# Optimization experiments

Measured on AMD Instinct MI355X. Metric: run time of the kernel, lower is better.

## Reference

```python
import jax, jax.numpy as jnp
import numpy as np

B, T, D = 2, 2048, 1024
H, G, K = 16, 4, 64          # num_heads, num_kv_heads, head_dim
R = H // G                   # GQA repeat factor
F = 4096                     # mlp_dim
EPS = 1e-6


def rms_norm(x, scale, eps=EPS):
    var = jnp.mean(x.astype(jnp.float32) ** 2, axis=-1, keepdims=True)
    normed = x * jax.lax.rsqrt(var + eps)
    return (scale * normed).astype(x.dtype)


def apply_rope(x_BTHK, sin_BTK, cos_BTK):
    half = x_BTHK.shape[-1] // 2
    x1, x2 = x_BTHK[..., :half], x_BTHK[..., half:]
    s = sin_BTK[:, :, None, :]
    c = cos_BTK[:, :, None, :]
    return jnp.concatenate([x1 * c - x2 * s, x2 * c + x1 * s], axis=-1).astype(x_BTHK.dtype)


def setup_inputs() -> dict:
    key = jax.random.key(0)
    ks = jax.random.split(key, 12)
    hidden_BTD = jax.random.normal(ks[0], (B, T, D), jnp.float32)
    # rope tables: realistic sin/cos of position*inv_freq
    inv_freq = 1.0 / (10000.0 ** (jnp.arange(K // 2, dtype=jnp.float32) / (K // 2)))
    ang = jnp.arange(T, dtype=jnp.float32)[:, None] * inv_freq[None, :]  # [T, K/2]
    sin_BTK = jnp.broadcast_to(jnp.sin(ang)[None], (B, T, K // 2))
    cos_BTK = jnp.broadcast_to(jnp.cos(ang)[None], (B, T, K // 2))
    mask = jnp.broadcast_to(jnp.tril(jnp.ones((T, T), bool))[None], (B, T, T))
    sc = 1.0 / np.sqrt(D)
    scf = 1.0 / np.sqrt(F)
    return {
        "hidden_BTD": hidden_BTD, "sin_BTK": sin_BTK, "cos_BTK": cos_BTK, "mask": mask,
        "ln1_scale": jnp.ones((D,), jnp.float32),
        "ln2_scale": jnp.ones((D,), jnp.float32),
        "qn_scale": jnp.ones((K,), jnp.float32),
        "kn_scale": jnp.ones((K,), jnp.float32),
        "q_w": jax.random.normal(ks[1], (D, H * K), jnp.float32) * sc,
        "k_w": jax.random.normal(ks[2], (D, G * K), jnp.float32) * sc,
        "v_w": jax.random.normal(ks[3], (D, G * K), jnp.float32) * sc,
        "o_w": jax.random.normal(ks[4], (H * K, D), jnp.float32) * sc,
        "gate_w": jax.random.normal(ks[5], (D, F), jnp.float32) * sc,
        "up_w": jax.random.normal(ks[6], (D, F), jnp.float32) * sc,
        "down_w": jax.random.normal(ks[7], (F, D), jnp.float32) * scf,
    }


def reference(hidden_BTD, sin_BTK, cos_BTK, mask, ln1_scale, ln2_scale,
              qn_scale, kn_scale, q_w, k_w, v_w, o_w, gate_w, up_w, down_w):
    x = rms_norm(hidden_BTD, ln1_scale)
    q = rms_norm((x @ q_w).reshape(B, T, H, K), qn_scale)
    k = rms_norm((x @ k_w).reshape(B, T, G, K), kn_scale)
    v = (x @ v_w).reshape(B, T, G, K)
    q = apply_rope(q, sin_BTK, cos_BTK)
    k = apply_rope(k, sin_BTK, cos_BTK)
    q_BTGRK = q.reshape(B, T, G, R, K)
    scale = K ** (-0.5)
    logits = jnp.einsum('BTGRK,BSGK->BTSGR', q_BTGRK, k) * scale
    neg = float(jnp.finfo(logits.dtype).min)
    logits = jnp.where(mask[:, :, :, None, None], logits, neg)
    weights = jax.nn.softmax(logits.astype(jnp.float32), axis=2).astype(logits.dtype)
    attn = jnp.einsum('BTSGR,BSGK->BTGRK', weights, v).reshape(B, T, H * K)
    hidden_BTD = hidden_BTD + attn @ o_w
    y = rms_norm(hidden_BTD, ln2_scale)
    ff = (jax.nn.silu(y @ gate_w) * (y @ up_w)) @ down_w
    return hidden_BTD + ff
```

## Files before the change

kernel.cpp:

```cpp
#include <hip/hip_runtime.h>
#include <hip/hip_bf16.h>

#define EPSF 1e-6f
constexpr int Bsz  = 2;
constexpr int Tseq = 2048;
constexpr int Dmod = 1024;
constexpr int Hh   = 16;
constexpr int Gg   = 4;
constexpr int Ff   = 4096;
constexpr int Mrows = Bsz * Tseq;

typedef __attribute__((ext_vector_type(8))) short bf16x8;
typedef __attribute__((ext_vector_type(4))) float f32x4;
typedef unsigned short u16;

__device__ inline u16 f2bf(float x) {
    union { float f; unsigned u; } v; v.f = x;
    unsigned r = v.u + 0x7fff + ((v.u >> 16) & 1);
    return (u16)(r >> 16);
}
__device__ inline float bf2f(u16 h) {
    union { unsigned u; float f; } v; v.u = ((unsigned)h) << 16; return v.f;
}

__device__ __forceinline__ void async_copy16(const u16* g, u16* l) {
    __builtin_amdgcn_global_load_lds(
        (const __attribute__((address_space(1))) void*)g,
        (__attribute__((address_space(3))) void*)l, 16, 0, 0);
}


template <int LO>
__global__ __launch_bounds__(256) void wprep_kernel(
    const float* __restrict__ W, u16* __restrict__ Th, u16* __restrict__ Tl,
    int Kd, int N)
{
    __shared__ float tile[32][33];
    const int n0 = blockIdx.x * 32, k0 = blockIdx.y * 32;
    const int r = threadIdx.x >> 3, c4 = (threadIdx.x & 7) * 4;
    const float4 v = *reinterpret_cast<const float4*>(&W[(size_t)(k0 + r) * N + n0 + c4]);
    tile[r][c4 + 0] = v.x; tile[r][c4 + 1] = v.y;
    tile[r][c4 + 2] = v.z; tile[r][c4 + 3] = v.w;
    __syncthreads();
    const int nl = threadIdx.x >> 3, kq = (threadIdx.x & 7) * 4;
    float x0 = tile[kq + 0][nl], x1 = tile[kq + 1][nl];
    float x2 = tile[kq + 2][nl], x3 = tile[kq + 3][nl];
    ushort4 h;
    h.x = f2bf(x0); h.y = f2bf(x1); h.z = f2bf(x2); h.w = f2bf(x3);
    *reinterpret_cast<ushort4*>(&Th[(size_t)(n0 + nl) * Kd + k0 + kq]) = h;
    if (LO) {
        ushort4 l;
        l.x = f2bf(x0 - bf2f(h.x)); l.y = f2bf(x1 - bf2f(h.y));
        l.z = f2bf(x2 - bf2f(h.z)); l.w = f2bf(x3 - bf2f(h.w));
        *reinterpret_cast<ushort4*>(&Tl[(size_t)(n0 + nl) * Kd + k0 + kq]) = l;
    }
}

__global__ __launch_bounds__(256) void wprep_qkv_kernel(
    const float* __restrict__ q_w, const float* __restrict__ k_w,
    const float* __restrict__ v_w, u16* __restrict__ QKVT)
{
    const int nx = blockIdx.x;
    const float* W; int N, n0s, drow;
    if (nx < 32)      { W = q_w; N = 1024; n0s = nx * 32;        drow = nx * 32; }
    else if (nx < 40) { W = k_w; N = 256;  n0s = (nx - 32) * 32; drow = 1024 + (nx - 32) * 32; }
    else              { W = v_w; N = 256;  n0s = (nx - 40) * 32; drow = 1280 + (nx - 40) * 32; }
    const int k0 = blockIdx.y * 32;
    __shared__ float tile[32][33];
    const int r = threadIdx.x >> 3, c4 = (threadIdx.x & 7) * 4;
    const float4 v = *reinterpret_cast<const float4*>(&W[(size_t)(k0 + r) * N + n0s + c4]);
    tile[r][c4 + 0] = v.x; tile[r][c4 + 1] = v.y;
    tile[r][c4 + 2] = v.z; tile[r][c4 + 3] = v.w;
    __syncthreads();
    const int nl = threadIdx.x >> 3, kq = (threadIdx.x & 7) * 4;
    ushort4 h;
    h.x = f2bf(tile[kq + 0][nl]); h.y = f2bf(tile[kq + 1][nl]);
    h.z = f2bf(tile[kq + 2][nl]); h.w = f2bf(tile[kq + 3][nl]);
    *reinterpret_cast<ushort4*>(&QKVT[(size_t)(drow + nl) * 1024 + k0 + kq]) = h;
}

__global__ __launch_bounds__(256) void wprep_gu_kernel(
    const float* __restrict__ gate_w, const float* __restrict__ up_w,
    u16* __restrict__ GTh, u16* __restrict__ UTh)
{
    const float* W = blockIdx.z ? up_w : gate_w;
    u16* T = blockIdx.z ? UTh : GTh;
    const int n0 = blockIdx.x * 32, k0 = blockIdx.y * 32;
    __shared__ float tile[32][33];
    const int r = threadIdx.x >> 3, c4 = (threadIdx.x & 7) * 4;
    const float4 v = *reinterpret_cast<const float4*>(&W[(size_t)(k0 + r) * 4096 + n0 + c4]);
    tile[r][c4 + 0] = v.x; tile[r][c4 + 1] = v.y;
    tile[r][c4 + 2] = v.z; tile[r][c4 + 3] = v.w;
    __syncthreads();
    const int nl = threadIdx.x >> 3, kq = (threadIdx.x & 7) * 4;
    ushort4 h;
    h.x = f2bf(tile[kq + 0][nl]); h.y = f2bf(tile[kq + 1][nl]);
    h.z = f2bf(tile[kq + 2][nl]); h.w = f2bf(tile[kq + 3][nl]);
    *reinterpret_cast<ushort4*>(&T[(size_t)(n0 + nl) * 1024 + k0 + kq]) = h;
}

template <int LO>
__global__ __launch_bounds__(256) void rmsnorm_split_kernel(
    const float* __restrict__ x, const float* __restrict__ scale,
    u16* __restrict__ oh, u16* __restrict__ ol)
{
    const int row = blockIdx.x;
    const int tid = threadIdx.x;
    const float4 v = reinterpret_cast<const float4*>(x + (size_t)row * Dmod)[tid];
    float ss = v.x * v.x + v.y * v.y + v.z * v.z + v.w * v.w;
    #pragma unroll
    for (int off = 32; off; off >>= 1) ss += __shfl_xor(ss, off, 64);
    __shared__ float part[4];
    if ((tid & 63) == 0) part[tid >> 6] = ss;
    __syncthreads();
    const float tot = part[0] + part[1] + part[2] + part[3];
    const float rstd = rsqrtf(tot * (1.0f / Dmod) + EPSF);
    const float4 sc = reinterpret_cast<const float4*>(scale)[tid];
    float o0 = v.x * rstd * sc.x, o1 = v.y * rstd * sc.y;
    float o2 = v.z * rstd * sc.z, o3 = v.w * rstd * sc.w;
    ushort4 h;
    h.x = f2bf(o0); h.y = f2bf(o1); h.z = f2bf(o2); h.w = f2bf(o3);
    *reinterpret_cast<ushort4*>(&oh[(size_t)row * Dmod + tid * 4]) = h;
    if (LO) {
        ushort4 l;
        l.x = f2bf(o0 - bf2f(h.x)); l.y = f2bf(o1 - bf2f(h.y));
        l.z = f2bf(o2 - bf2f(h.z)); l.w = f2bf(o3 - bf2f(h.w));
        *reinterpret_cast<ushort4*>(&ol[(size_t)row * Dmod + tid * 4]) = l;
    }
}

template <int ASPLIT, int BSPLIT, int RES>
__global__ __launch_bounds__(256, 2) void mfma_gemm_kernel(
    const u16* __restrict__ Ah, const u16* __restrict__ Al,
    const u16* __restrict__ Bh, const u16* __restrict__ Bl,
    const float* __restrict__ res, float* __restrict__ C,
    int M, int N, int Kd)
{
    __shared__ u16 As_h[128 * 32];
    __shared__ u16 As_l[128 * 32];
    __shared__ u16 Bs_h[128 * 32];
    __shared__ u16 Bs_l[128 * 32];

    const int tid = threadIdx.x;
    const int lane = tid & 63, wave = tid >> 6;
    const int wm = (wave >> 1) * 64, wn = (wave & 1) * 64;
    const int m0 = blockIdx.y * 128, n0 = blockIdx.x * 128;
    const int fm = lane & 15, quad = lane >> 4;
    const int fsw = (fm >> 1) & 3;
    const int fcol = ((quad ^ fsw) * 8);

    f32x4 acc[4][4];
    #pragma unroll
    for (int i = 0; i < 4; ++i)
        #pragma unroll
        for (int j = 0; j < 4; ++j) acc[i][j] = (f32x4){0.f, 0.f, 0.f, 0.f};

    const int lrow = lane >> 2;
    const int lchunk = lane & 3;
    const int schunk = lchunk ^ ((lrow >> 1) & 3);

    for (int k0 = 0; k0 < Kd; k0 += 32) {
        __syncthreads();
        #pragma unroll
        for (int p = 0; p < 2; ++p) {
            const int row = wave * 32 + p * 16 + lrow;
            const size_t ga = (size_t)(m0 + row) * Kd + k0 + schunk * 8;
            const size_t gb = (size_t)(n0 + row) * Kd + k0 + schunk * 8;
            const int ls = row * 32 + lchunk * 8;
            async_copy16(&Ah[ga], &As_h[ls]);
            if (ASPLIT) async_copy16(&Al[ga], &As_l[ls]);
            async_copy16(&Bh[gb], &Bs_h[ls]);
            if (BSPLIT) async_copy16(&Bl[gb], &Bs_l[ls]);
        }
        __syncthreads();

        bf16x8 ah[4], al[4], bh[4], bl[4];
        #pragma unroll
        for (int t = 0; t < 4; ++t) {
            const int ra = (wm + t * 16 + fm) * 32 + fcol;
            const int rb = (wn + t * 16 + fm) * 32 + fcol;
            ah[t] = *reinterpret_cast<const bf16x8*>(&As_h[ra]);
            bh[t] = *reinterpret_cast<const bf16x8*>(&Bs_h[rb]);
            if (ASPLIT) al[t] = *reinterpret_cast<const bf16x8*>(&As_l[ra]);
            if (BSPLIT) bl[t] = *reinterpret_cast<const bf16x8*>(&Bs_l[rb]);
        }
        #pragma unroll
        for (int mt = 0; mt < 4; ++mt)
            #pragma unroll
            for (int nt = 0; nt < 4; ++nt) {
                acc[mt][nt] = __builtin_amdgcn_mfma_f32_16x16x32_bf16(
                    ah[mt], bh[nt], acc[mt][nt], 0, 0, 0);
                if (BSPLIT)
                    acc[mt][nt] = __builtin_amdgcn_mfma_f32_16x16x32_bf16(
                        ah[mt], bl[nt], acc[mt][nt], 0, 0, 0);
                if (ASPLIT)
                    acc[mt][nt] = __builtin_amdgcn_mfma_f32_16x16x32_bf16(
                        al[mt], bh[nt], acc[mt][nt], 0, 0, 0);
            }
    }

    const int cr = (lane >> 4) * 4, cn = lane & 15;
    #pragma unroll
    for (int mt = 0; mt < 4; ++mt)
        #pragma unroll
        for (int nt = 0; nt < 4; ++nt)
            #pragma unroll
            for (int r = 0; r < 4; ++r) {
                const int gm = m0 + wm + mt * 16 + cr + r;
                const int gn = n0 + wn + nt * 16 + cn;
                float v = acc[mt][nt][r];
                if (RES) v += res[(size_t)gm * N + gn];
                C[(size_t)gm * N + gn] = v;
            }
}

__global__ __launch_bounds__(256, 2) void qkv_fused_kernel(
    const u16* __restrict__ Ah, const u16* __restrict__ Bh,
    const float* __restrict__ qn, const float* __restrict__ kn,
    const float* __restrict__ sinp, const float* __restrict__ cosp,
    u16* __restrict__ Qbh, u16* __restrict__ Qbl,
    u16* __restrict__ Kbh, u16* __restrict__ Kbl,
    u16* __restrict__ Vbh, u16* __restrict__ Vbl)
{
    __shared__ u16 As_h[128 * 32];
    __shared__ u16 Bs_h[128 * 32];

    const int Kd = 1024;
    const int tid = threadIdx.x;
    const int lane = tid & 63, wave = tid >> 6;
    const int wm = (wave >> 1) * 64, wn = (wave & 1) * 64;
    const int m0 = blockIdx.y * 128, n0 = blockIdx.x * 128;
    const int fm = lane & 15, quad = lane >> 4;
    const int fsw = (fm >> 1) & 3;
    const int fcol = ((quad ^ fsw) * 8);

    f32x4 acc[4][4];
    #pragma unroll
    for (int i = 0; i < 4; ++i)
        #pragma unroll
        for (int j = 0; j < 4; ++j) acc[i][j] = (f32x4){0.f, 0.f, 0.f, 0.f};

    const int lrow = lane >> 2;
    const int lchunk = lane & 3;
    const int schunk = lchunk ^ ((lrow >> 1) & 3);

    for (int k0 = 0; k0 < Kd; k0 += 32) {
        __syncthreads();
        #pragma unroll
        for (int p = 0; p < 2; ++p) {
            const int row = wave * 32 + p * 16 + lrow;
            const size_t ga = (size_t)(m0 + row) * Kd + k0 + schunk * 8;
            const size_t gb = (size_t)(n0 + row) * Kd + k0 + schunk * 8;
            const int ls = row * 32 + lchunk * 8;
            async_copy16(&Ah[ga], &As_h[ls]);
            async_copy16(&Bh[gb], &Bs_h[ls]);
        }
        __syncthreads();

        bf16x8 ah[4], bh[4];
        #pragma unroll
        for (int t = 0; t < 4; ++t) {
            ah[t] = *reinterpret_cast<const bf16x8*>(&As_h[(wm + t * 16 + fm) * 32 + fcol]);
            bh[t] = *reinterpret_cast<const bf16x8*>(&Bs_h[(wn + t * 16 + fm) * 32 + fcol]);
        }
        #pragma unroll
        for (int mt = 0; mt < 4; ++mt)
            #pragma unroll
            for (int nt = 0; nt < 4; ++nt)
                acc[mt][nt] = __builtin_amdgcn_mfma_f32_16x16x32_bf16(
                    ah[mt], bh[nt], acc[mt][nt], 0, 0, 0);
    }

    const int gn0 = n0 + wn;
    const int l15 = lane & 15;

    if (gn0 < 1280) {
        const bool isQ = (gn0 < 1024);
        const float* nsc = isQ ? qn : kn;
        const float osc = isQ ? 0.125f : 1.0f;
        u16* __restrict__ oh = isQ ? Qbh : Kbh;
        u16* __restrict__ ol = isQ ? Qbl : Kbl;
        const int rowstride = isQ ? 1024 : 256;
        const int colbase = isQ ? gn0 : gn0 - 1024;
        float sc[4];
        #pragma unroll
        for (int nt = 0; nt < 4; ++nt) sc[nt] = nsc[nt * 16 + l15];

        #pragma unroll
        for (int mt = 0; mt < 4; ++mt)
            #pragma unroll
            for (int r = 0; r < 4; ++r) {
                const int bt = m0 + wm + mt * 16 + quad * 4 + r;
                float v[4];
                #pragma unroll
                for (int nt = 0; nt < 4; ++nt) v[nt] = acc[mt][nt][r];
                float ss = v[0] * v[0] + v[1] * v[1] + v[2] * v[2] + v[3] * v[3];
                #pragma unroll
                for (int off = 1; off < 16; off <<= 1)
                    ss += __shfl_xor(ss, off, 16);
                const float rstd = rsqrtf(ss * (1.0f / 64.0f) + EPSF);
                float nv[4];
                #pragma unroll
                for (int nt = 0; nt < 4; ++nt) nv[nt] = v[nt] * rstd * sc[nt];
                const float s0 = sinp[bt * 32 + l15];
                const float c0 = cosp[bt * 32 + l15];
                const float s1 = sinp[bt * 32 + 16 + l15];
                const float c1 = cosp[bt * 32 + 16 + l15];
                float o[4];
                o[0] = (nv[0] * c0 - nv[2] * s0) * osc;
                o[1] = (nv[1] * c1 - nv[3] * s1) * osc;
                o[2] = (nv[2] * c0 + nv[0] * s0) * osc;
                o[3] = (nv[3] * c1 + nv[1] * s1) * osc;
                #pragma unroll
                for (int nt = 0; nt < 4; ++nt) {
                    const size_t off = (size_t)bt * rowstride + colbase + nt * 16 + l15;
                    const u16 hi = f2bf(o[nt]);
                    oh[off] = hi;
                    ol[off] = f2bf(o[nt] - bf2f(hi));
                }
            }
    } else {
        const int colbase = gn0 - 1280;
        #pragma unroll
        for (int mt = 0; mt < 4; ++mt)
            #pragma unroll
            for (int r = 0; r < 4; ++r) {
                const int bt = m0 + wm + mt * 16 + quad * 4 + r;
                #pragma unroll
                for (int nt = 0; nt < 4; ++nt) {
                    const float v = acc[mt][nt][r];
                    const size_t off = (size_t)bt * 256 + colbase + nt * 16 + l15;
                    const u16 hi = f2bf(v);
                    Vbh[off] = hi;
                    Vbl[off] = f2bf(v - bf2f(hi));
                }
            }
    }
}

__global__ __launch_bounds__(256) void vtrans_bf16_kernel(
    const u16* __restrict__ Vbh, const u16* __restrict__ Vbl,
    u16* __restrict__ Vth, u16* __restrict__ Vtl)
{
    __shared__ u16 th[64 * 66];
    __shared__ u16 tl[64 * 66];
    const int t0 = blockIdx.x * 64;
    const int bg = blockIdx.y;
    const int b = bg >> 2, g = bg & 3;
    const int tid = threadIdx.x;

    const int row = tid >> 2;
    const int cc = (tid & 3) * 16;
    const size_t src = (size_t)(b * Tseq + t0 + row) * 256 + g * 64 + cc;
    *reinterpret_cast<uint4*>(&th[row * 66 + cc]) =
        *reinterpret_cast<const uint4*>(&Vbh[src]);
    *reinterpret_cast<uint4*>(&th[row * 66 + cc + 8]) =
        *reinterpret_cast<const uint4*>(&Vbh[src + 8]);
    *reinterpret_cast<uint4*>(&tl[row * 66 + cc]) =
        *reinterpret_cast<const uint4*>(&Vbl[src]);
    *reinterpret_cast<uint4*>(&tl[row * 66 + cc + 8]) =
        *reinterpret_cast<const uint4*>(&Vbl[src + 8]);
    __syncthreads();

    const int d = tid >> 2;
    const int tq = (tid & 3) * 16;
    u16 oh[16], ol[16];
    #pragma unroll
    for (int i = 0; i < 16; ++i) {
        oh[i] = th[(tq + i) * 66 + d];
        ol[i] = tl[(tq + i) * 66 + d];
    }
    const size_t dst = (size_t)(bg * 64 + d) * Tseq + t0 + tq;
    *reinterpret_cast<uint4*>(&Vth[dst])     = *reinterpret_cast<uint4*>(&oh[0]);
    *reinterpret_cast<uint4*>(&Vth[dst + 8]) = *reinterpret_cast<uint4*>(&oh[8]);
    *reinterpret_cast<uint4*>(&Vtl[dst])     = *reinterpret_cast<uint4*>(&ol[0]);
    *reinterpret_cast<uint4*>(&Vtl[dst + 8]) = *reinterpret_cast<uint4*>(&ol[8]);
}

__global__ __launch_bounds__(256, 2) void mfma_gateup_kernel(
    const u16* __restrict__ Ah, const u16* __restrict__ Al,
    const u16* __restrict__ Bg, const u16* __restrict__ Bu,
    u16* __restrict__ FF, int M, int N, int Kd)
{
    __shared__ u16 As_h[128 * 32];
    __shared__ u16 As_l[128 * 32];
    __shared__ u16 Gs[64 * 32];
    __shared__ u16 Us[64 * 32];

    const int tid = threadIdx.x;
    const int lane = tid & 63, wave = tid >> 6;
    const int wm = (wave >> 1) * 64, wn = (wave & 1) * 32;
    const int m0 = blockIdx.y * 128, n0 = blockIdx.x * 64;
    const int fm = lane & 15, quad = lane >> 4;
    const int fsw = (fm >> 1) & 3;
    const int fcol = ((quad ^ fsw) * 8);

    f32x4 accg[4][2], accu[4][2];
    #pragma unroll
    for (int i = 0; i < 4; ++i)
        #pragma unroll
        for (int j = 0; j < 2; ++j) {
            accg[i][j] = (f32x4){0.f, 0.f, 0.f, 0.f};
            accu[i][j] = (f32x4){0.f, 0.f, 0.f, 0.f};
        }

    const int lrow = lane >> 2;
    const int lchunk = lane & 3;
    const int schunk = lchunk ^ ((lrow >> 1) & 3);

    for (int k0 = 0; k0 < Kd; k0 += 32) {
        __syncthreads();
        #pragma unroll
        for (int p = 0; p < 2; ++p) {
            const int row = p * 64 + wave * 16 + lrow;
            const size_t ga = (size_t)(m0 + row) * Kd + k0 + schunk * 8;
            const int ls = row * 32 + lchunk * 8;
            async_copy16(&Ah[ga], &As_h[ls]);
            async_copy16(&Al[ga], &As_l[ls]);
        }
        {
            const int row = wave * 16 + lrow;
            const size_t gb = (size_t)(n0 + row) * Kd + k0 + schunk * 8;
            const int ls = row * 32 + lchunk * 8;
            async_copy16(&Bg[gb], &Gs[ls]);
            async_copy16(&Bu[gb], &Us[ls]);
        }
        __syncthreads();

        bf16x8 a_h[4], a_l[4], g_f[2], u_f[2];
        #pragma unroll
        for (int t = 0; t < 4; ++t) {
            const int ra = (wm + t * 16 + fm) * 32 + fcol;
            a_h[t] = *reinterpret_cast<const bf16x8*>(&As_h[ra]);
            a_l[t] = *reinterpret_cast<const bf16x8*>(&As_l[ra]);
        }
        #pragma unroll
        for (int j = 0; j < 2; ++j) {
            const int rb = (wn + j * 16 + fm) * 32 + fcol;
            g_f[j] = *reinterpret_cast<const bf16x8*>(&Gs[rb]);
            u_f[j] = *reinterpret_cast<const bf16x8*>(&Us[rb]);
        }
        #pragma unroll
        for (int mt = 0; mt < 4; ++mt)
            #pragma unroll
            for (int nt = 0; nt < 2; ++nt) {
                accg[mt][nt] = __builtin_amdgcn_mfma_f32_16x16x32_bf16(
                    a_h[mt], g_f[nt], accg[mt][nt], 0, 0, 0);
                accg[mt][nt] = __builtin_amdgcn_mfma_f32_16x16x32_bf16(
                    a_l[mt], g_f[nt], accg[mt][nt], 0, 0, 0);
                accu[mt][nt] = __builtin_amdgcn_mfma_f32_16x16x32_bf16(
                    a_h[mt], u_f[nt], accu[mt][nt], 0, 0, 0);
                accu[mt][nt] = __builtin_amdgcn_mfma_f32_16x16x32_bf16(
                    a_l[mt], u_f[nt], accu[mt][nt], 0, 0, 0);
            }
    }

    const int cr = (lane >> 4) * 4, cn = lane & 15;
    #pragma unroll
    for (int mt = 0; mt < 4; ++mt)
        #pragma unroll
        for (int nt = 0; nt < 2; ++nt)
            #pragma unroll
            for (int r = 0; r < 4; ++r) {
                const int gm = m0 + wm + mt * 16 + cr + r;
                const int gn = n0 + wn + nt * 16 + cn;
                const float g = accg[mt][nt][r];
                const float ff = (g / (1.0f + __expf(-g))) * accu[mt][nt][r];
                FF[(size_t)gm * N + gn] = f2bf(ff);
            }
}

__global__ __launch_bounds__(256) void attn_mfma_kernel(
    const u16* __restrict__ Qh, const u16* __restrict__ Ql,
    const u16* __restrict__ Kh, const u16* __restrict__ Kl,
    const u16* __restrict__ Vth, const u16* __restrict__ Vtl,
    u16* __restrict__ AOh, u16* __restrict__ AOl)
{
    __shared__ u16 KsH[64 * 72];
    __shared__ u16 KsL[64 * 72];
    __shared__ u16 VsH[64 * 72];
    __shared__ u16 VsL[64 * 72];
    __shared__ u16 Ps[4][16 * 72];

    const int tid = threadIdx.x;
    const int wave = tid >> 6, lane = tid & 63;
    const int l15 = lane & 15, quad = lane >> 4;

    const int bg = blockIdx.x & 7;
    const int b = bg >> 2, g = bg & 3;
    const int win = 127 - (blockIdx.x >> 3);
    const int t0 = win * 16;
    const int h = g * 4 + wave;

    bf16x8 qh[2], ql[2];
    {
        const size_t qrow = (size_t)(b * Tseq + t0 + l15) * 1024 + h * 64;
        #pragma unroll
        for (int ks = 0; ks < 2; ++ks) {
            qh[ks] = *reinterpret_cast<const bf16x8*>(&Qh[qrow + ks * 32 + quad * 8]);
            ql[ks] = *reinterpret_cast<const bf16x8*>(&Ql[qrow + ks * 32 + quad * 8]);
        }
    }

    const int srow = tid >> 2;
    const int scol = (tid & 3) * 16;
    const size_t kgb = (size_t)(b * Tseq) * 256 + g * 64 + scol;
    const size_t vgb = (size_t)(bg * 64 + srow) * Tseq + scol;

    const int nit = t0 / 64 + 1;

    uint4 ck0, ck1, cl0, cl1, cv0, cv1, cw0, cw1;
    {
        const size_t ka = kgb + (size_t)srow * 256;
        ck0 = *reinterpret_cast<const uint4*>(&Kh[ka]);
        ck1 = *reinterpret_cast<const uint4*>(&Kh[ka + 8]);
        cl0 = *reinterpret_cast<const uint4*>(&Kl[ka]);
        cl1 = *reinterpret_cast<const uint4*>(&Kl[ka + 8]);
        cv0 = *reinterpret_cast<const uint4*>(&Vth[vgb]);
        cv1 = *reinterpret_cast<const uint4*>(&Vth[vgb + 8]);
        cw0 = *reinterpret_cast<const uint4*>(&Vtl[vgb]);
        cw1 = *reinterpret_cast<const uint4*>(&Vtl[vgb + 8]);
    }

    f32x4 oacc[4];
    #pragma unroll
    for (int nt = 0; nt < 4; ++nt) oacc[nt] = (f32x4){0.f, 0.f, 0.f, 0.f};
    float m_r[4], l_r[4];
    #pragma unroll
    for (int r = 0; r < 4; ++r) { m_r[r] = -1e30f; l_r[r] = 0.0f; }

    u16* psw = &Ps[wave][0];
    const int lb = srow * 72 + scol;

    for (int it = 0; it < nit; ++it) {
        const int s0 = it * 64;
        const bool diag = (it == nit - 1);

        __syncthreads();
        *reinterpret_cast<uint4*>(&KsH[lb])     = ck0;
        *reinterpret_cast<uint4*>(&KsH[lb + 8]) = ck1;
        *reinterpret_cast<uint4*>(&KsL[lb])     = cl0;
        *reinterpret_cast<uint4*>(&KsL[lb + 8]) = cl1;
        *reinterpret_cast<uint4*>(&VsH[lb])     = cv0;
        *reinterpret_cast<uint4*>(&VsH[lb + 8]) = cv1;
        *reinterpret_cast<uint4*>(&VsL[lb])     = cw0;
        *reinterpret_cast<uint4*>(&VsL[lb + 8]) = cw1;
        if (it + 1 < nit) {
            const size_t ka = kgb + (size_t)(s0 + 64 + srow) * 256;
            ck0 = *reinterpret_cast<const uint4*>(&Kh[ka]);
            ck1 = *reinterpret_cast<const uint4*>(&Kh[ka + 8]);
            cl0 = *reinterpret_cast<const uint4*>(&Kl[ka]);
            cl1 = *reinterpret_cast<const uint4*>(&Kl[ka + 8]);
            const size_t va = vgb + s0 + 64;
            cv0 = *reinterpret_cast<const uint4*>(&Vth[va]);
            cv1 = *reinterpret_cast<const uint4*>(&Vth[va + 8]);
            cw0 = *reinterpret_cast<const uint4*>(&Vtl[va]);
            cw1 = *reinterpret_cast<const uint4*>(&Vtl[va + 8]);
        }
        __syncthreads();

        f32x4 sacc[4];
        #pragma unroll
        for (int nt = 0; nt < 4; ++nt) sacc[nt] = (f32x4){0.f, 0.f, 0.f, 0.f};

        #pragma unroll
        for (int ks = 0; ks < 2; ++ks) {
            bf16x8 kfh[4], kfl[4];
            #pragma unroll
            for (int nt = 0; nt < 4; ++nt) {
                const int a = (nt * 16 + l15) * 72 + ks * 32 + quad * 8;
                kfh[nt] = *reinterpret_cast<const bf16x8*>(&KsH[a]);
                kfl[nt] = *reinterpret_cast<const bf16x8*>(&KsL[a]);
            }
            #pragma unroll
            for (int nt = 0; nt < 4; ++nt) {
                sacc[nt] = __builtin_amdgcn_mfma_f32_16x16x32_bf16(qh[ks], kfh[nt], sacc[nt], 0, 0, 0);
                sacc[nt] = __builtin_amdgcn_mfma_f32_16x16x32_bf16(ql[ks], kfh[nt], sacc[nt], 0, 0, 0);
                sacc[nt] = __builtin_amdgcn_mfma_f32_16x16x32_bf16(qh[ks], kfl[nt], sacc[nt], 0, 0, 0);
            }
        }

        if (diag) {
            #pragma unroll
            for (int nt = 0; nt < 4; ++nt) {
                const int sg = s0 + nt * 16 + l15;
                #pragma unroll
                for (int r = 0; r < 4; ++r)
                    if (sg > t0 + quad * 4 + r) sacc[nt][r] = -1e30f;
            }
        }

        #pragma unroll
        for (int r = 0; r < 4; ++r) {
            float mx = fmaxf(fmaxf(sacc[0][r], sacc[1][r]),
                             fmaxf(sacc[2][r], sacc[3][r]));
            #pragma unroll
            for (int off = 1; off < 16; off <<= 1)
                mx = fmaxf(mx, __shfl_xor(mx, off, 16));
            const float mnew = fmaxf(m_r[r], mx);
            const float alpha = __expf(m_r[r] - mnew);
            m_r[r] = mnew;

            float rs = 0.0f;
            #pragma unroll
            for (int nt = 0; nt < 4; ++nt) {
                const float p = __expf(sacc[nt][r] - mnew);
                sacc[nt][r] = p;
                rs += p;
            }
            #pragma unroll
            for (int off = 1; off < 16; off <<= 1)
                rs += __shfl_xor(rs, off, 16);
            l_r[r] = l_r[r] * alpha + rs;
            #pragma unroll
            for (int nt = 0; nt < 4; ++nt) oacc[nt][r] *= alpha;
            #pragma unroll
            for (int nt = 0; nt < 4; ++nt)
                psw[(quad * 4 + r) * 72 + nt * 16 + l15] = f2bf(sacc[nt][r]);
        }

        #pragma unroll
        for (int ks = 0; ks < 2; ++ks) {
            const bf16x8 pa = *reinterpret_cast<const bf16x8*>(
                &psw[l15 * 72 + ks * 32 + quad * 8]);
            bf16x8 vfh[4], vfl[4];
            #pragma unroll
            for (int nt = 0; nt < 4; ++nt) {
                const int a = (nt * 16 + l15) * 72 + ks * 32 + quad * 8;
                vfh[nt] = *reinterpret_cast<const bf16x8*>(&VsH[a]);
                vfl[nt] = *reinterpret_cast<const bf16x8*>(&VsL[a]);
            }
            #pragma unroll
            for (int nt = 0; nt < 4; ++nt) {
                oacc[nt] = __builtin_amdgcn_mfma_f32_16x16x32_bf16(pa, vfh[nt], oacc[nt], 0, 0, 0);
                oacc[nt] = __builtin_amdgcn_mfma_f32_16x16x32_bf16(pa, vfl[nt], oacc[nt], 0, 0, 0);
            }
        }
    }

    #pragma unroll
    for (int r = 0; r < 4; ++r) {
        const float inv = 1.0f / l_r[r];
        const size_t orow = (size_t)(b * Tseq + t0 + quad * 4 + r) * 1024 + h * 64;
        #pragma unroll
        for (int nt = 0; nt < 4; ++nt) {
            const float o = oacc[nt][r] * inv;
            const u16 hi = f2bf(o);
            AOh[orow + nt * 16 + l15] = hi;
            AOl[orow + nt * 16 + l15] = f2bf(o - bf2f(hi));
        }
    }
}

extern "C" void kernel_launch(void* const* d_in, const int* in_sizes, int n_in,
                              void* d_out, int out_size, void* d_ws,
                              size_t ws_size, hipStream_t stream)
{
    const float* hidden = (const float*)d_in[0];
    const float* sinp   = (const float*)d_in[1];
    const float* cosp   = (const float*)d_in[2];
    const float* ln1    = (const float*)d_in[4];
    const float* ln2    = (const float*)d_in[5];
    const float* qn     = (const float*)d_in[6];
    const float* kn     = (const float*)d_in[7];
    const float* q_w    = (const float*)d_in[8];
    const float* k_w    = (const float*)d_in[9];
    const float* v_w    = (const float*)d_in[10];
    const float* o_w    = (const float*)d_in[11];
    const float* gate_w = (const float*)d_in[12];
    const float* up_w   = (const float*)d_in[13];
    const float* down_w = (const float*)d_in[14];
    float* out = (float*)d_out;

    char* base = (char*)d_ws;
    u16*   OTh  = (u16*)(base);
    u16*   OTl  = (u16*)(base + 2097152);
    u16*   GTh  = (u16*)(base + 4194304);
    u16*   UTh  = (u16*)(base + 12582912);
    u16*   DTh  = (u16*)(base + 20971520);
    u16*   QKVT = (u16*)(base + 29360128);
    u16*   Xh   = (u16*)(base + 32505856);
    u16*   Qbh  = (u16*)(base + 40894464);
    u16*   Qbl  = (u16*)(base + 49283072);
    u16*   Kbh  = (u16*)(base + 57671680);
    u16*   Kbl  = (u16*)(base + 59768832);
    u16*   Vbh  = (u16*)(base + 61865984);
    u16*   Vbl  = (u16*)(base + 63963136);
    u16*   Vth  = (u16*)(base + 66060288);
    u16*   Vtl  = (u16*)(base + 68157440);
    u16*   AOh  = (u16*)(base + 70254592);
    u16*   AOl  = (u16*)(base + 78643200);
    u16*   FFh  = (u16*)(base + 87031808);

    float* H2 = (float*)Qbh;
    u16*   Yh = Kbh;
    u16*   Yl = Vth;

    wprep_qkv_kernel<<<dim3(48, 32), 256, 0, stream>>>(q_w, k_w, v_w, QKVT);
    wprep_kernel<1><<<dim3(32, 32), 256, 0, stream>>>(o_w, OTh, OTl, 1024, 1024);
    wprep_gu_kernel<<<dim3(128, 32, 2), 256, 0, stream>>>(gate_w, up_w, GTh, UTh);
    wprep_kernel<0><<<dim3(32, 128), 256, 0, stream>>>(down_w, DTh, nullptr, 4096, 1024);

    rmsnorm_split_kernel<0><<<Mrows, 256, 0, stream>>>(hidden, ln1, Xh, nullptr);

    qkv_fused_kernel<<<dim3(12, 32), 256, 0, stream>>>(
        Xh, QKVT, qn, kn, sinp, cosp, Qbh, Qbl, Kbh, Kbl, Vbh, Vbl);

    vtrans_bf16_kernel<<<dim3(Tseq / 64, Bsz * Gg), 256, 0, stream>>>(
        Vbh, Vbl, Vth, Vtl);

    attn_mfma_kernel<<<Bsz * Gg * (Tseq / 16), 256, 0, stream>>>(
        Qbh, Qbl, Kbh, Kbl, Vth, Vtl, AOh, AOl);

    mfma_gemm_kernel<1, 1, 1><<<dim3(8, 32), 256, 0, stream>>>(
        AOh, AOl, OTh, OTl, hidden, H2, Mrows, Dmod, 1024);

    rmsnorm_split_kernel<1><<<Mrows, 256, 0, stream>>>(H2, ln2, Yh, Yl);

    mfma_gateup_kernel<<<dim3(Ff / 64, Mrows / 128), 256, 0, stream>>>(
        Yh, Yl, GTh, UTh, FFh, Mrows, Ff, 1024);

    mfma_gemm_kernel<0, 0, 1><<<dim3(8, 32), 256, 0, stream>>>(
        FFh, nullptr, DTh, nullptr, H2, out, Mrows, Dmod, 4096);
}
```

Measured before the change: 543.8 us.

## Merge weight-prep kernels, write V transposed from QKV, process two query strips per attention block

Folds the four weight conversion kernels into one launch over a flat block index, removing launch overhead. The QKV GEMM epilogue now writes V directly in the transposed layout, dropping the separate V transpose kernel and its round trip through memory. The attention kernel handles two 16-row query strips per block so each staged K/V tile is reused twice, halving the grid and K/V traffic. In exchange it raises register pressure in attention and uses strided 8-byte stores for V.

```diff
diff --git a/kernel.cpp b/kernel.cpp
--- a/kernel.cpp
+++ b/kernel.cpp
@@ -30,13 +30,48 @@
 }
 
 
-template <int LO>
-__global__ __launch_bounds__(256) void wprep_kernel(
-    const float* __restrict__ W, u16* __restrict__ Th, u16* __restrict__ Tl,
-    int Kd, int N)
+__global__ __launch_bounds__(256) void wprep_all_kernel(
+    const float* __restrict__ q_w, const float* __restrict__ k_w,
+    const float* __restrict__ v_w, const float* __restrict__ o_w,
+    const float* __restrict__ gate_w, const float* __restrict__ up_w,
+    const float* __restrict__ down_w,
+    u16* __restrict__ QKVT, u16* __restrict__ OTh, u16* __restrict__ OTl,
+    u16* __restrict__ GTh, u16* __restrict__ UTh, u16* __restrict__ DTh)
 {
+    const int bx = blockIdx.x;
+    const float* W; u16* Th; u16* Tl = nullptr;
+    int N, Kd, ntile, ktile, drow;
+    if (bx < 1024) {
+        W = q_w; N = 1024; Kd = 1024; ntile = bx & 31; ktile = bx >> 5;
+        Th = QKVT; drow = ntile * 32;
+    } else if (bx < 1280) {
+        const int i = bx - 1024;
+        W = k_w; N = 256; Kd = 1024; ntile = i & 7; ktile = i >> 3;
+        Th = QKVT; drow = 1024 + ntile * 32;
+    } else if (bx < 1536) {
+        const int i = bx - 1280;
+        W = v_w; N = 256; Kd = 1024; ntile = i & 7; ktile = i >> 3;
+        Th = QKVT; drow = 1280 + ntile * 32;
+    } else if (bx < 2560) {
+        const int i = bx - 1536;
+        W = o_w; N = 1024; Kd = 1024; ntile = i & 31; ktile = i >> 5;
+        Th = OTh; Tl = OTl; drow = ntile * 32;
+    } else if (bx < 6656) {
+        const int i = bx - 2560;
+        W = gate_w; N = 4096; Kd = 1024; ntile = i & 127; ktile = i >> 7;
+        Th = GTh; drow = ntile * 32;
+    } else if (bx < 10752) {
+        const int i = bx - 6656;
+        W = up_w; N = 4096; Kd = 1024; ntile = i & 127; ktile = i >> 7;
+        Th = UTh; drow = ntile * 32;
+    } else {
+        const int i = bx - 10752;
+        W = down_w; N = 1024; Kd = 4096; ntile = i & 31; ktile = i >> 5;
+        Th = DTh; drow = ntile * 32;
+    }
+    const int n0 = ntile * 32, k0 = ktile * 32;
+
     __shared__ float tile[32][33];
-    const int n0 = blockIdx.x * 32, k0 = blockIdx.y * 32;
     const int r = threadIdx.x >> 3, c4 = (threadIdx.x & 7) * 4;
     const float4 v = *reinterpret_cast<const float4*>(&W[(size_t)(k0 + r) * N + n0 + c4]);
     tile[r][c4 + 0] = v.x; tile[r][c4 + 1] = v.y;
@@ -47,56 +82,13 @@
     float x2 = tile[kq + 2][nl], x3 = tile[kq + 3][nl];
     ushort4 h;
     h.x = f2bf(x0); h.y = f2bf(x1); h.z = f2bf(x2); h.w = f2bf(x3);
-    *reinterpret_cast<ushort4*>(&Th[(size_t)(n0 + nl) * Kd + k0 + kq]) = h;
-    if (LO) {
+    *reinterpret_cast<ushort4*>(&Th[(size_t)(drow + nl) * Kd + k0 + kq]) = h;
+    if (Tl) {
         ushort4 l;
         l.x = f2bf(x0 - bf2f(h.x)); l.y = f2bf(x1 - bf2f(h.y));
         l.z = f2bf(x2 - bf2f(h.z)); l.w = f2bf(x3 - bf2f(h.w));
-        *reinterpret_cast<ushort4*>(&Tl[(size_t)(n0 + nl) * Kd + k0 + kq]) = l;
-    }
-}
-
-__global__ __launch_bounds__(256) void wprep_qkv_kernel(
-    const float* __restrict__ q_w, const float* __restrict__ k_w,
-    const float* __restrict__ v_w, u16* __restrict__ QKVT)
-{
-    const int nx = blockIdx.x;
-    const float* W; int N, n0s, drow;
-    if (nx < 32)      { W = q_w; N = 1024; n0s = nx * 32;        drow = nx * 32; }
-    else if (nx < 40) { W = k_w; N = 256;  n0s = (nx - 32) * 32; drow = 1024 + (nx - 32) * 32; }
-    else              { W = v_w; N = 256;  n0s = (nx - 40) * 32; drow = 1280 + (nx - 40) * 32; }
-    const int k0 = blockIdx.y * 32;
-    __shared__ float tile[32][33];
-    const int r = threadIdx.x >> 3, c4 = (threadIdx.x & 7) * 4;
-    const float4 v = *reinterpret_cast<const float4*>(&W[(size_t)(k0 + r) * N + n0s + c4]);
-    tile[r][c4 + 0] = v.x; tile[r][c4 + 1] = v.y;
-    tile[r][c4 + 2] = v.z; tile[r][c4 + 3] = v.w;
-    __syncthreads();
-    const int nl = threadIdx.x >> 3, kq = (threadIdx.x & 7) * 4;
-    ushort4 h;
-    h.x = f2bf(tile[kq + 0][nl]); h.y = f2bf(tile[kq + 1][nl]);
-    h.z = f2bf(tile[kq + 2][nl]); h.w = f2bf(tile[kq + 3][nl]);
-    *reinterpret_cast<ushort4*>(&QKVT[(size_t)(drow + nl) * 1024 + k0 + kq]) = h;
-}
-
-__global__ __launch_bounds__(256) void wprep_gu_kernel(
-    const float* __restrict__ gate_w, const float* __restrict__ up_w,
-    u16* __restrict__ GTh, u16* __restrict__ UTh)
-{
-    const float* W = blockIdx.z ? up_w : gate_w;
-    u16* T = blockIdx.z ? UTh : GTh;
-    const int n0 = blockIdx.x * 32, k0 = blockIdx.y * 32;
-    __shared__ float tile[32][33];
-    const int r = threadIdx.x >> 3, c4 = (threadIdx.x & 7) * 4;
-    const float4 v = *reinterpret_cast<const float4*>(&W[(size_t)(k0 + r) * 4096 + n0 + c4]);
-    tile[r][c4 + 0] = v.x; tile[r][c4 + 1] = v.y;
-    tile[r][c4 + 2] = v.z; tile[r][c4 + 3] = v.w;
-    __syncthreads();
-    const int nl = threadIdx.x >> 3, kq = (threadIdx.x & 7) * 4;
-    ushort4 h;
-    h.x = f2bf(tile[kq + 0][nl]); h.y = f2bf(tile[kq + 1][nl]);
-    h.z = f2bf(tile[kq + 2][nl]); h.w = f2bf(tile[kq + 3][nl]);
-    *reinterpret_cast<ushort4*>(&T[(size_t)(n0 + nl) * 1024 + k0 + kq]) = h;
+        *reinterpret_cast<ushort4*>(&Tl[(size_t)(drow + nl) * Kd + k0 + kq]) = l;
+    }
 }
 
 template <int LO>
@@ -220,7 +212,7 @@
     const float* __restrict__ sinp, const float* __restrict__ cosp,
     u16* __restrict__ Qbh, u16* __restrict__ Qbl,
     u16* __restrict__ Kbh, u16* __restrict__ Kbl,
-    u16* __restrict__ Vbh, u16* __restrict__ Vbl)
+    u16* __restrict__ Vth, u16* __restrict__ Vtl)
 {
     __shared__ u16 As_h[128 * 32];
     __shared__ u16 Bs_h[128 * 32];
@@ -320,61 +312,25 @@
                 }
             }
     } else {
-        const int colbase = gn0 - 1280;
+        const int g = (gn0 - 1280) >> 6;
+        const int b = (m0 + wm) >> 11;
+        const int tb = ((m0 + wm) & 2047) + quad * 4;
         #pragma unroll
         for (int mt = 0; mt < 4; ++mt)
             #pragma unroll
-            for (int r = 0; r < 4; ++r) {
-                const int bt = m0 + wm + mt * 16 + quad * 4 + r;
-                #pragma unroll
-                for (int nt = 0; nt < 4; ++nt) {
-                    const float v = acc[mt][nt][r];
-                    const size_t off = (size_t)bt * 256 + colbase + nt * 16 + l15;
-                    const u16 hi = f2bf(v);
-                    Vbh[off] = hi;
-                    Vbl[off] = f2bf(v - bf2f(hi));
-                }
+            for (int nt = 0; nt < 4; ++nt) {
+                const float v0 = acc[mt][nt][0], v1 = acc[mt][nt][1];
+                const float v2 = acc[mt][nt][2], v3 = acc[mt][nt][3];
+                ushort4 hv, lv;
+                hv.x = f2bf(v0); hv.y = f2bf(v1); hv.z = f2bf(v2); hv.w = f2bf(v3);
+                lv.x = f2bf(v0 - bf2f(hv.x)); lv.y = f2bf(v1 - bf2f(hv.y));
+                lv.z = f2bf(v2 - bf2f(hv.z)); lv.w = f2bf(v3 - bf2f(hv.w));
+                const size_t off =
+                    ((size_t)((b * 4 + g) * 64 + nt * 16 + l15)) * Tseq + tb + mt * 16;
+                *reinterpret_cast<ushort4*>(&Vth[off]) = hv;
+                *reinterpret_cast<ushort4*>(&Vtl[off]) = lv;
             }
     }
-}
-
-__global__ __launch_bounds__(256) void vtrans_bf16_kernel(
-    const u16* __restrict__ Vbh, const u16* __restrict__ Vbl,
-    u16* __restrict__ Vth, u16* __restrict__ Vtl)
-{
-    __shared__ u16 th[64 * 66];
-    __shared__ u16 tl[64 * 66];
-    const int t0 = blockIdx.x * 64;
-    const int bg = blockIdx.y;
-    const int b = bg >> 2, g = bg & 3;
-    const int tid = threadIdx.x;
-
-    const int row = tid >> 2;
-    const int cc = (tid & 3) * 16;
-    const size_t src = (size_t)(b * Tseq + t0 + row) * 256 + g * 64 + cc;
-    *reinterpret_cast<uint4*>(&th[row * 66 + cc]) =
-        *reinterpret_cast<const uint4*>(&Vbh[src]);
-    *reinterpret_cast<uint4*>(&th[row * 66 + cc + 8]) =
-        *reinterpret_cast<const uint4*>(&Vbh[src + 8]);
-    *reinterpret_cast<uint4*>(&tl[row * 66 + cc]) =
-        *reinterpret_cast<const uint4*>(&Vbl[src]);
-    *reinterpret_cast<uint4*>(&tl[row * 66 + cc + 8]) =
-        *reinterpret_cast<const uint4*>(&Vbl[src + 8]);
-    __syncthreads();
-
-    const int d = tid >> 2;
-    const int tq = (tid & 3) * 16;
-    u16 oh[16], ol[16];
-    #pragma unroll
-    for (int i = 0; i < 16; ++i) {
-        oh[i] = th[(tq + i) * 66 + d];
-        ol[i] = tl[(tq + i) * 66 + d];
-    }
-    const size_t dst = (size_t)(bg * 64 + d) * Tseq + t0 + tq;
-    *reinterpret_cast<uint4*>(&Vth[dst])     = *reinterpret_cast<uint4*>(&oh[0]);
-    *reinterpret_cast<uint4*>(&Vth[dst + 8]) = *reinterpret_cast<uint4*>(&oh[8]);
-    *reinterpret_cast<uint4*>(&Vtl[dst])     = *reinterpret_cast<uint4*>(&ol[0]);
-    *reinterpret_cast<uint4*>(&Vtl[dst + 8]) = *reinterpret_cast<uint4*>(&ol[8]);
 }
 
 __global__ __launch_bounds__(256, 2) void mfma_gateup_kernel(
@@ -470,6 +426,91 @@
             }
 }
 
+__device__ __forceinline__ void attn_strip_step(
+    const bf16x8* qh, const bf16x8* ql,
+    const u16* KsH, const u16* KsL, const u16* VsH, const u16* VsL,
+    u16* psw, int s0, int t0, int l15, int quad,
+    f32x4* oacc, float* m_r, float* l_r)
+{
+    f32x4 sacc[4];
+    #pragma unroll
+    for (int nt = 0; nt < 4; ++nt) sacc[nt] = (f32x4){0.f, 0.f, 0.f, 0.f};
+
+    #pragma unroll
+    for (int ks = 0; ks < 2; ++ks) {
+        bf16x8 kfh[4], kfl[4];
+        #pragma unroll
+        for (int nt = 0; nt < 4; ++nt) {
+            const int a = (nt * 16 + l15) * 72 + ks * 32 + quad * 8;
+            kfh[nt] = *reinterpret_cast<const bf16x8*>(&KsH[a]);
+            kfl[nt] = *reinterpret_cast<const bf16x8*>(&KsL[a]);
+        }
+        #pragma unroll
+        for (int nt = 0; nt < 4; ++nt) {
+            sacc[nt] = __builtin_amdgcn_mfma_f32_16x16x32_bf16(qh[ks], kfh[nt], sacc[nt], 0, 0, 0);
+            sacc[nt] = __builtin_amdgcn_mfma_f32_16x16x32_bf16(ql[ks], kfh[nt], sacc[nt], 0, 0, 0);
+            sacc[nt] = __builtin_amdgcn_mfma_f32_16x16x32_bf16(qh[ks], kfl[nt], sacc[nt], 0, 0, 0);
+        }
+    }
+
+    if (s0 + 63 > t0) {
+        #pragma unroll
+        for (int nt = 0; nt < 4; ++nt) {
+            const int sg = s0 + nt * 16 + l15;
+            #pragma unroll
+            for (int r = 0; r < 4; ++r)
+                if (sg > t0 + quad * 4 + r) sacc[nt][r] = -1e30f;
+        }
+    }
+
+    #pragma unroll
+    for (int r = 0; r < 4; ++r) {
+        float mx = fmaxf(fmaxf(sacc[0][r], sacc[1][r]),
+                         fmaxf(sacc[2][r], sacc[3][r]));
+        #pragma unroll
+        for (int off = 1; off < 16; off <<= 1)
+            mx = fmaxf(mx, __shfl_xor(mx, off, 16));
+        const float mnew = fmaxf(m_r[r], mx);
+        const float alpha = __expf(m_r[r] - mnew);
+        m_r[r] = mnew;
+
+        float rs = 0.0f;
+        #pragma unroll
+        for (int nt = 0; nt < 4; ++nt) {
+            const float p = __expf(sacc[nt][r] - mnew);
+            sacc[nt][r] = p;
+            rs += p;
+        }
+        #pragma unroll
+        for (int off = 1; off < 16; off <<= 1)
+            rs += __shfl_xor(rs, off, 16);
+        l_r[r] = l_r[r] * alpha + rs;
+        #pragma unroll
+        for (int nt = 0; nt < 4; ++nt) oacc[nt][r] *= alpha;
+        #pragma unroll
+        for (int nt = 0; nt < 4; ++nt)
+            psw[(quad * 4 + r) * 72 + nt * 16 + l15] = f2bf(sacc[nt][r]);
+    }
+
+    #pragma unroll
+    for (int ks = 0; ks < 2; ++ks) {
+        const bf16x8 pa = *reinterpret_cast<const bf16x8*>(
+            &psw[l15 * 72 + ks * 32 + quad * 8]);
+        bf16x8 vfh[4], vfl[4];
+        #pragma unroll
+        for (int nt = 0; nt < 4; ++nt) {
+            const int a = (nt * 16 + l15) * 72 + ks * 32 + quad * 8;
+            vfh[nt] = *reinterpret_cast<const bf16x8*>(&VsH[a]);
+            vfl[nt] = *reinterpret_cast<const bf16x8*>(&VsL[a]);
+        }
+        #pragma unroll
+        for (int nt = 0; nt < 4; ++nt) {
+            oacc[nt] = __builtin_amdgcn_mfma_f32_16x16x32_bf16(pa, vfh[nt], oacc[nt], 0, 0, 0);
+            oacc[nt] = __builtin_amdgcn_mfma_f32_16x16x32_bf16(pa, vfl[nt], oacc[nt], 0, 0, 0);
+        }
+    }
+}
+
 __global__ __launch_bounds__(256) void attn_mfma_kernel(
     const u16* __restrict__ Qh, const u16* __restrict__ Ql,
     const u16* __restrict__ Kh, const u16* __restrict__ Kl,
@@ -488,17 +529,21 @@
 
     const int bg = blockIdx.x & 7;
     const int b = bg >> 2, g = bg & 3;
-    const int win = 127 - (blockIdx.x >> 3);
-    const int t0 = win * 16;
+    const int wp = 63 - (blockIdx.x >> 3);
+    const int t0a = wp * 32;
+    const int t0b = t0a + 16;
     const int h = g * 4 + wave;
 
-    bf16x8 qh[2], ql[2];
+    bf16x8 qha[2], qla[2], qhb[2], qlb[2];
     {
-        const size_t qrow = (size_t)(b * Tseq + t0 + l15) * 1024 + h * 64;
+        const size_t ra = (size_t)(b * Tseq + t0a + l15) * 1024 + h * 64;
+        const size_t rb = (size_t)(b * Tseq + t0b + l15) * 1024 + h * 64;
         #pragma unroll
         for (int ks = 0; ks < 2; ++ks) {
-            qh[ks] = *reinterpret_cast<const bf16x8*>(&Qh[qrow + ks * 32 + quad * 8]);
-            ql[ks] = *reinterpret_cast<const bf16x8*>(&Ql[qrow + ks * 32 + quad * 8]);
+            qha[ks] = *reinterpret_cast<const bf16x8*>(&Qh[ra + ks * 32 + quad * 8]);
+            qla[ks] = *reinterpret_cast<const bf16x8*>(&Ql[ra + ks * 32 + quad * 8]);
+            qhb[ks] = *reinterpret_cast<const bf16x8*>(&Qh[rb + ks * 32 + quad * 8]);
+            qlb[ks] = *reinterpret_cast<const bf16x8*>(&Ql[rb + ks * 32 + quad * 8]);
         }
     }
 
@@ -507,7 +552,7 @@
     const size_t kgb = (size_t)(b * Tseq) * 256 + g * 64 + scol;
     const size_t vgb = (size_t)(bg * 64 + srow) * Tseq + scol;
 
-    const int nit = t0 / 64 + 1;
+    const int nit = t0b / 64 + 1;
 
     uint4 ck0, ck1, cl0, cl1, cv0, cv1, cw0, cw1;
     {
@@ -522,29 +567,34 @@
         cw1 = *reinterpret_cast<const uint4*>(&Vtl[vgb + 8]);
     }
 
-    f32x4 oacc[4];
-    #pragma unroll
-    for (int nt = 0; nt < 4; ++nt) oacc[nt] = (f32x4){0.f, 0.f, 0.f, 0.f};
-    float m_r[4], l_r[4];
-    #pragma unroll
-    for (int r = 0; r < 4; ++r) { m_r[r] = -1e30f; l_r[r] = 0.0f; }
+    f32x4 oa[4], ob[4];
+    #pragma unroll
+    for (int nt = 0; nt < 4; ++nt) {
+        oa[nt] = (f32x4){0.f, 0.f, 0.f, 0.f};
+        ob[nt] = (f32x4){0.f, 0.f, 0.f, 0.f};
+    }
+    float ma[4], la[4], mb[4], lb[4];
+    #pragma unroll
+    for (int r = 0; r < 4; ++r) {
+        ma[r] = -1e30f; la[r] = 0.0f;
+        mb[r] = -1e30f; lb[r] = 0.0f;
+    }
 
     u16* psw = &Ps[wave][0];
-    const int lb = srow * 72 + scol;
+    const int lbo = srow * 72 + scol;
 
     for (int it = 0; it < nit; ++it) {
         const int s0 = it * 64;
-        const bool diag = (it == nit - 1);
 
         __syncthreads();
-        *reinterpret_cast<uint4*>(&KsH[lb])     = ck0;
-        *reinterpret_cast<uint4*>(&KsH[lb + 8]) = ck1;
-        *reinterpret_cast<uint4*>(&KsL[lb])     = cl0;
-        *reinterpret_cast<uint4*>(&KsL[lb + 8]) = cl1;
-        *reinterpret_cast<uint4*>(&VsH[lb])     = cv0;
-        *reinterpret_cast<uint4*>(&VsH[lb + 8]) = cv1;
-        *reinterpret_cast<uint4*>(&VsL[lb])     = cw0;
-        *reinterpret_cast<uint4*>(&VsL[lb + 8]) = cw1;
+        *reinterpret_cast<uint4*>(&KsH[lbo])     = ck0;
+        *reinterpret_cast<uint4*>(&KsH[lbo + 8]) = ck1;
+        *reinterpret_cast<uint4*>(&KsL[lbo])     = cl0;
+        *reinterpret_cast<uint4*>(&KsL[lbo + 8]) = cl1;
+        *reinterpret_cast<uint4*>(&VsH[lbo])     = cv0;
+        *reinterpret_cast<uint4*>(&VsH[lbo + 8]) = cv1;
+        *reinterpret_cast<uint4*>(&VsL[lbo])     = cw0;
+        *reinterpret_cast<uint4*>(&VsL[lbo + 8]) = cw1;
         if (it + 1 < nit) {
             const size_t ka = kgb + (size_t)(s0 + 64 + srow) * 256;
             ck0 = *reinterpret_cast<const uint4*>(&Kh[ka]);
@@ -559,95 +609,29 @@
         }
         __syncthreads();
 
-        f32x4 sacc[4];
-        #pragma unroll
-        for (int nt = 0; nt < 4; ++nt) sacc[nt] = (f32x4){0.f, 0.f, 0.f, 0.f};
-
-        #pragma unroll
-        for (int ks = 0; ks < 2; ++ks) {
-            bf16x8 kfh[4], kfl[4];
-            #pragma unroll
-            for (int nt = 0; nt < 4; ++nt) {
-                const int a = (nt * 16 + l15) * 72 + ks * 32 + quad * 8;
-                kfh[nt] = *reinterpret_cast<const bf16x8*>(&KsH[a]);
-                kfl[nt] = *reinterpret_cast<const bf16x8*>(&KsL[a]);
-            }
-            #pragma unroll
-            for (int nt = 0; nt < 4; ++nt) {
-                sacc[nt] = __builtin_amdgcn_mfma_f32_16x16x32_bf16(qh[ks], kfh[nt], sacc[nt], 0, 0, 0);
-                sacc[nt] = __builtin_amdgcn_mfma_f32_16x16x32_bf16(ql[ks], kfh[nt], sacc[nt], 0, 0, 0);
-                sacc[nt] = __builtin_amdgcn_mfma_f32_16x16x32_bf16(qh[ks], kfl[nt], sacc[nt], 0, 0, 0);
-            }
-        }
-
-        if (diag) {
-            #pragma unroll
-            for (int nt = 0; nt < 4; ++nt) {
-                const int sg = s0 + nt * 16 + l15;
-                #pragma unroll
-                for (int r = 0; r < 4; ++r)
-                    if (sg > t0 + quad * 4 + r) sacc[nt][r] = -1e30f;
-            }
-        }
-
-        #pragma unroll
-        for (int r = 0; r < 4; ++r) {
-            float mx = fmaxf(fmaxf(sacc[0][r], sacc[1][r]),
-                             fmaxf(sacc[2][r], sacc[3][r]));
-            #pragma unroll
-            for (int off = 1; off < 16; off <<= 1)
-                mx = fmaxf(mx, __shfl_xor(mx, off, 16));
-            const float mnew = fmaxf(m_r[r], mx);
-            const float alpha = __expf(m_r[r] - mnew);
-            m_r[r] = mnew;
-
-            float rs = 0.0f;
-            #pragma unroll
-            for (int nt = 0; nt < 4; ++nt) {
-                const float p = __expf(sacc[nt][r] - mnew);
-                sacc[nt][r] = p;
-                rs += p;
-            }
-            #pragma unroll
-            for (int off = 1; off < 16; off <<= 1)
-                rs += __shfl_xor(rs, off, 16);
-            l_r[r] = l_r[r] * alpha + rs;
-            #pragma unroll
-            for (int nt = 0; nt < 4; ++nt) oacc[nt][r] *= alpha;
-            #pragma unroll
-            for (int nt = 0; nt < 4; ++nt)
-                psw[(quad * 4 + r) * 72 + nt * 16 + l15] = f2bf(sacc[nt][r]);
-        }
-
-        #pragma unroll
-        for (int ks = 0; ks < 2; ++ks) {
-            const bf16x8 pa = *reinterpret_cast<const bf16x8*>(
-                &psw[l15 * 72 + ks * 32 + quad * 8]);
-            bf16x8 vfh[4], vfl[4];
-            #pragma unroll
-            for (int nt = 0; nt < 4; ++nt) {
-                const int a = (nt * 16 + l15) * 72 + ks * 32 + quad * 8;
-                vfh[nt] = *reinterpret_cast<const bf16x8*>(&VsH[a]);
-                vfl[nt] = *reinterpret_cast<const bf16x8*>(&VsL[a]);
-            }
-            #pragma unroll
-            for (int nt = 0; nt < 4; ++nt) {
-                oacc[nt] = __builtin_amdgcn_mfma_f32_16x16x32_bf16(pa, vfh[nt], oacc[nt], 0, 0, 0);
-                oacc[nt] = __builtin_amdgcn_mfma_f32_16x16x32_bf16(pa, vfl[nt], oacc[nt], 0, 0, 0);
-            }
-        }
+        if (s0 <= t0a + 15)
+            attn_strip_step(qha, qla, KsH, KsL, VsH, VsL, psw,
+                            s0, t0a, l15, quad, oa, ma, la);
+        attn_strip_step(qhb, qlb, KsH, KsL, VsH, VsL, psw,
+                        s0, t0b, l15, quad, ob, mb, lb);
     }
 
     #pragma unroll
     for (int r = 0; r < 4; ++r) {
-        const float inv = 1.0f / l_r[r];
-        const size_t orow = (size_t)(b * Tseq + t0 + quad * 4 + r) * 1024 + h * 64;
+        const float inva = 1.0f / la[r];
+        const float invb = 1.0f / lb[r];
+        const size_t rowa = (size_t)(b * Tseq + t0a + quad * 4 + r) * 1024 + h * 64;
+        const size_t rowb = (size_t)(b * Tseq + t0b + quad * 4 + r) * 1024 + h * 64;
         #pragma unroll
         for (int nt = 0; nt < 4; ++nt) {
-            const float o = oacc[nt][r] * inv;
-            const u16 hi = f2bf(o);
-            AOh[orow + nt * 16 + l15] = hi;
-            AOl[orow + nt * 16 + l15] = f2bf(o - bf2f(hi));
+            const float o1 = oa[nt][r] * inva;
+            const float o2 = ob[nt][r] * invb;
+            const u16 h1 = f2bf(o1);
+            const u16 h2 = f2bf(o2);
+            AOh[rowa + nt * 16 + l15] = h1;
+            AOl[rowa + nt * 16 + l15] = f2bf(o1 - bf2f(h1));
+            AOh[rowb + nt * 16 + l15] = h2;
+            AOl[rowb + nt * 16 + l15] = f2bf(o2 - bf2f(h2));
         }
     }
 }
@@ -684,32 +668,26 @@
     u16*   Qbl  = (u16*)(base + 49283072);
     u16*   Kbh  = (u16*)(base + 57671680);
     u16*   Kbl  = (u16*)(base + 59768832);
-    u16*   Vbh  = (u16*)(base + 61865984);
-    u16*   Vbl  = (u16*)(base + 63963136);
-    u16*   Vth  = (u16*)(base + 66060288);
-    u16*   Vtl  = (u16*)(base + 68157440);
-    u16*   AOh  = (u16*)(base + 70254592);
-    u16*   AOl  = (u16*)(base + 78643200);
-    u16*   FFh  = (u16*)(base + 87031808);
+    u16*   Vth  = (u16*)(base + 61865984);
+    u16*   Vtl  = (u16*)(base + 63963136);
+    u16*   AOh  = (u16*)(base + 66060288);
+    u16*   AOl  = (u16*)(base + 74448896);
+    u16*   FFh  = (u16*)(base + 82837504);
 
     float* H2 = (float*)Qbh;
     u16*   Yh = Kbh;
-    u16*   Yl = Vth;
-
-    wprep_qkv_kernel<<<dim3(48, 32), 256, 0, stream>>>(q_w, k_w, v_w, QKVT);
-    wprep_kernel<1><<<dim3(32, 32), 256, 0, stream>>>(o_w, OTh, OTl, 1024, 1024);
-    wprep_gu_kernel<<<dim3(128, 32, 2), 256, 0, stream>>>(gate_w, up_w, GTh, UTh);
-    wprep_kernel<0><<<dim3(32, 128), 256, 0, stream>>>(down_w, DTh, nullptr, 4096, 1024);
+    u16*   Yl = AOh;
+
+    wprep_all_kernel<<<14848, 256, 0, stream>>>(
+        q_w, k_w, v_w, o_w, gate_w, up_w, down_w,
+        QKVT, OTh, OTl, GTh, UTh, DTh);
 
     rmsnorm_split_kernel<0><<<Mrows, 256, 0, stream>>>(hidden, ln1, Xh, nullptr);
 
     qkv_fused_kernel<<<dim3(12, 32), 256, 0, stream>>>(
-        Xh, QKVT, qn, kn, sinp, cosp, Qbh, Qbl, Kbh, Kbl, Vbh, Vbl);
-
-    vtrans_bf16_kernel<<<dim3(Tseq / 64, Bsz * Gg), 256, 0, stream>>>(
-        Vbh, Vbl, Vth, Vtl);
-
-    attn_mfma_kernel<<<Bsz * Gg * (Tseq / 16), 256, 0, stream>>>(
+        Xh, QKVT, qn, kn, sinp, cosp, Qbh, Qbl, Kbh, Kbl, Vth, Vtl);
+
+    attn_mfma_kernel<<<Bsz * Gg * (Tseq / 32), 256, 0, stream>>>(
         Qbh, Qbl, Kbh, Kbl, Vth, Vtl, AOh, AOl);
 
     mfma_gemm_kernel<1, 1, 1><<<dim3(8, 32), 256, 0, stream>>>(
```

After: 570.2 us. 4.9% more time.
